# Kernel optimization log

Hardware: AMD Instinct MI355X
Metric: run time of the kernel (lower is better)

## Reference

```python
import jax, jax.numpy as jnp
import numpy as np

N_NODES = 100000


def _gcn_layer(x, src, dst, ew, norm_s, norm_d, W, b):
    # DGL GraphConv with edge weights, norm='both':
    # h_v = D_in(v)^-1/2 * sum_{(u,v) in E} w_uv * D_out(u)^-1/2 * x_u; then Linear.
    m = (x * norm_s[:, None])[src] * ew[:, None]        # [E, d] gather + weight
    agg = jax.ops.segment_sum(m, dst, num_segments=N_NODES)  # [N, d] scatter-add
    return (agg * norm_d[:, None]) @ W + b


def setup_inputs() -> dict:
    key = jax.random.key(0)
    ks = jax.random.split(key, 12)
    N, E, D, C = N_NODES, 1600000, 64, 32
    inp = {
        "x": jax.random.normal(ks[0], (N, D), jnp.float32),
        "src": jax.random.randint(ks[1], (E,), 0, N, jnp.int64),
        "dst": jax.random.randint(ks[2], (E,), 0, N, jnp.int64),
        "ew": jax.random.uniform(ks[3], (E,), jnp.float32),
    }
    s = 1.0 / np.sqrt(D)
    for i, k in zip(range(1, 5), ks[4:8]):
        inp[f"W{i}"] = jax.random.normal(k, (D, D), jnp.float32) * s
        inp[f"b{i}"] = jnp.zeros((D,), jnp.float32)
    inp["Wr"] = jax.random.normal(ks[8], (D, D), jnp.float32) * s
    inp["br"] = jnp.zeros((D,), jnp.float32)
    inp["Wo"] = jax.random.normal(ks[9], (D, C), jnp.float32) * s
    inp["bo"] = jnp.zeros((C,), jnp.float32)
    return inp


def reference(x, src, dst, ew, W1, b1, W2, b2, W3, b3, W4, b4, Wr, br, Wo, bo):
    ones = jnp.ones(src.shape, x.dtype)
    deg_out = jnp.clip(jax.ops.segment_sum(ones, src, num_segments=N_NODES), 1.0)
    deg_in = jnp.clip(jax.ops.segment_sum(ones, dst, num_segments=N_NODES), 1.0)
    norm_s = deg_out ** -0.5
    norm_d = deg_in ** -0.5

    res = x @ Wr + br
    h = jax.nn.relu(_gcn_layer(x, src, dst, ew, norm_s, norm_d, W1, b1))
    h = jax.nn.relu(_gcn_layer(h, src, dst, ew, norm_s, norm_d, W2, b2))
    h = jax.nn.relu(_gcn_layer(h, src, dst, ew, norm_s, norm_d, W3, b3))
    h = _gcn_layer(h, src, dst, ew, norm_s, norm_d, W4, b4)
    h = jax.nn.relu(h + res)
    return h @ Wo + bo
```

## Files before the change

### kernel.cpp

```cpp
#include <hip/hip_runtime.h>

#define NN 100000
#define D 64
#define G 4
#define RS 25000
#define NC 64
#define NB (G*NC)

typedef short bf16x8 __attribute__((ext_vector_type(8)));
typedef float f32x4 __attribute__((ext_vector_type(4)));

__device__ __forceinline__ float bf2f_lo(unsigned w) { return __uint_as_float(w << 16); }
__device__ __forceinline__ float bf2f_hi(unsigned w) { return __uint_as_float(w & 0xffff0000u); }
__device__ __forceinline__ unsigned short f2bf(float f) {
    unsigned u = __float_as_uint(f);
    return (unsigned short)((u + 0x7fffu + ((u >> 16) & 1u)) >> 16);
}
__device__ __forceinline__ unsigned pack2(float a, float b) {
    return (unsigned)f2bf(a) | ((unsigned)f2bf(b) << 16);
}

__global__ __launch_bounds__(1024) void k_hist(const int* __restrict__ src,
                                               const int* __restrict__ dst,
                                               unsigned* __restrict__ part, int E) {
    __shared__ unsigned h[RS];
    int b = blockIdx.x, t = threadIdx.x;
    int g = b >> 6, c = b & 63;
    int lo = g * RS;
    for (int i = t; i < RS; i += 1024) h[i] = 0;
    __syncthreads();
    int e0 = (int)((((long long)c * E / NC)) & ~3LL);
    int e1 = (c == NC - 1) ? E : (int)((((long long)(c + 1) * E / NC)) & ~3LL);
    int m = (e1 - e0) & ~4095;
    for (int e = e0 + t * 4; e < e0 + m; e += 4096) {
        int4 s4 = *(const int4*)(src + e);
        int4 d4 = *(const int4*)(dst + e);
        int v;
        v = s4.x - lo; if ((unsigned)v < RS) atomicAdd(&h[v], 1u);
        v = s4.y - lo; if ((unsigned)v < RS) atomicAdd(&h[v], 1u);
        v = s4.z - lo; if ((unsigned)v < RS) atomicAdd(&h[v], 1u);
        v = s4.w - lo; if ((unsigned)v < RS) atomicAdd(&h[v], 1u);
        v = d4.x - lo; if ((unsigned)v < RS) atomicAdd(&h[v], 0x10000u);
        v = d4.y - lo; if ((unsigned)v < RS) atomicAdd(&h[v], 0x10000u);
        v = d4.z - lo; if ((unsigned)v < RS) atomicAdd(&h[v], 0x10000u);
        v = d4.w - lo; if ((unsigned)v < RS) atomicAdd(&h[v], 0x10000u);
    }
    for (int e = e0 + m + t; e < e1; e += 1024) {
        int v = src[e] - lo; if ((unsigned)v < RS) atomicAdd(&h[v], 1u);
        v = dst[e] - lo;     if ((unsigned)v < RS) atomicAdd(&h[v], 0x10000u);
    }
    __syncthreads();
    unsigned* pb = part + (size_t)b * RS;
    for (int i = t; i < RS; i += 1024) pb[i] = h[i];
}

__global__ __launch_bounds__(1024) void k_scan1m(const unsigned* __restrict__ part,
                                                 float* __restrict__ ns, float* __restrict__ nd,
                                                 int* __restrict__ rowptr,
                                                 int* __restrict__ bsum, int n) {
    __shared__ int lds[1024];
    int t = threadIdx.x;
    int i = blockIdx.x * 1024 + t;
    int sv = 0, dv = 0;
    if (i < n) {
        int g = i / RS, off = i - g * RS;
        const unsigned* p = part + (size_t)(g * NC) * RS + off;
        #pragma unroll 8
        for (int c = 0; c < NC; ++c) {
            unsigned v = p[(size_t)c * RS];
            sv += (int)(v & 0xffffu);
            dv += (int)(v >> 16);
        }
        ns[i] = rsqrtf(fmaxf((float)sv, 1.0f));
        nd[i] = rsqrtf(fmaxf((float)dv, 1.0f));
    }
    lds[t] = dv;
    __syncthreads();
    for (int off = 1; off < 1024; off <<= 1) {
        int v = lds[t];
        int a = (t >= off) ? lds[t - off] : 0;
        __syncthreads();
        lds[t] = v + a;
        __syncthreads();
    }
    if (t == 1023) bsum[blockIdx.x] = lds[1023];
    if (i < n) rowptr[i] = lds[t] - dv;
}

__global__ void k_scan3c(int* __restrict__ rowptr, const int* __restrict__ bsum,
                         const unsigned* __restrict__ part, int* __restrict__ cur_part,
                         int n, int E, int nb) {
    __shared__ int sbs[128];
    int t = threadIdx.x;
    if (t < 128) sbs[t] = (t < nb) ? bsum[t] : 0;
    __syncthreads();
    for (int off = 1; off < 128; off <<= 1) {
        int v = 0, a = 0;
        if (t < 128) { v = sbs[t]; if (t >= off) a = sbs[t - off]; }
        __syncthreads();
        if (t < 128) sbs[t] = v + a;
        __syncthreads();
    }
    int i = blockIdx.x * blockDim.x + t;
    if (i == 0) rowptr[n] = E;
    if (i >= n) return;
    int blk = i >> 10;
    int base = (blk > 0) ? sbs[blk - 1] : 0;
    int r = rowptr[i] + base;
    rowptr[i] = r;
    int g = i / RS, off = i - g * RS;
    const unsigned* p = part + (size_t)(g * NC) * RS + off;
    int* cp = cur_part + (size_t)(g * NC) * RS + off;
    int run = r;
    #pragma unroll 8
    for (int c = 0; c < NC; ++c) {
        cp[(size_t)c * RS] = run;
        run += (int)(p[(size_t)c * RS] >> 16);
    }
}

__global__ __launch_bounds__(1024) void k_fillsort(const int* __restrict__ src,
                                                   const int* __restrict__ dst,
                                                   const float* __restrict__ ew,
                                                   const int* __restrict__ cur_part,
                                                   int2* __restrict__ cw, int E) {
    __shared__ int cur[RS];
    int b = blockIdx.x, t = threadIdx.x;
    int g = b >> 6, c = b & 63;
    int lo = g * RS;
    const int* cp = cur_part + (size_t)b * RS;
    for (int i = t; i < RS; i += 1024) cur[i] = cp[i];
    __syncthreads();
    int e0 = (int)((((long long)c * E / NC)) & ~3LL);
    int e1 = (c == NC - 1) ? E : (int)((((long long)(c + 1) * E / NC)) & ~3LL);
    int m = (e1 - e0) & ~4095;
    for (int e = e0 + t * 4; e < e0 + m; e += 4096) {
        int4 s4 = *(const int4*)(src + e);
        int4 d4 = *(const int4*)(dst + e);
        float4 w4 = *(const float4*)(ew + e);
        int d;
        d = d4.x - lo; if ((unsigned)d < RS) { int p = atomicAdd(&cur[d], 1); cw[p] = make_int2(s4.x, __float_as_int(w4.x)); }
        d = d4.y - lo; if ((unsigned)d < RS) { int p = atomicAdd(&cur[d], 1); cw[p] = make_int2(s4.y, __float_as_int(w4.y)); }
        d = d4.z - lo; if ((unsigned)d < RS) { int p = atomicAdd(&cur[d], 1); cw[p] = make_int2(s4.z, __float_as_int(w4.z)); }
        d = d4.w - lo; if ((unsigned)d < RS) { int p = atomicAdd(&cur[d], 1); cw[p] = make_int2(s4.w, __float_as_int(w4.w)); }
    }
    for (int e = e0 + m + t; e < e1; e += 1024) {
        int d = dst[e] - lo;
        if ((unsigned)d < RS) {
            int p = atomicAdd(&cur[d], 1);
            cw[p] = make_int2(src[e], __float_as_int(ew[e]));
        }
    }
}

__global__ void k_scale(const float* __restrict__ x, const float* __restrict__ ns,
                        unsigned short* __restrict__ xsb, int n16) {
    int i = blockIdx.x * blockDim.x + threadIdx.x;
    if (i < n16) {
        float s = ns[i >> 4];
        float4 v = ((const float4*)x)[i];
        ((uint2*)xsb)[i] = make_uint2(pack2(v.x * s, v.y * s), pack2(v.z * s, v.w * s));
    }
}

template<bool LAST>
__global__ void k_gather(const int* __restrict__ rowptr, const int2* __restrict__ cw,
                         const unsigned short* __restrict__ tmat,
                         const float* __restrict__ nd, const float* __restrict__ ns,
                         const float* __restrict__ bias,
                         const unsigned short* __restrict__ resb,
                         unsigned short* __restrict__ outb, int n, int E) {
    int node = blockIdx.x * (blockDim.x >> 5) + (threadIdx.x >> 5);
    int lane = threadIdx.x & 31;
    if (node >= n) return;
    int g = lane >> 3;
    int h = lane & 7;
    int beg = rowptr[node], end = rowptr[node + 1];
    float a0=0,a1=0,a2=0,a3=0,a4=0,a5=0,a6=0,a7=0;
    float c0=0,c1=0,c2=0,c3=0,c4=0,c5=0,c6=0,c7=0;
    for (int base = beg; base < end; base += 16) {
        int eA = base + g;
        int eB = eA + 4;
        int eC = eA + 8;
        int eD = eA + 12;
        int2 cvA = cw[min(eA, E - 1)];
        int2 cvB = cw[min(eB, E - 1)];
        int2 cvC = cw[min(eC, E - 1)];
        int2 cvD = cw[min(eD, E - 1)];
        float wA = (eA < end) ? __int_as_float(cvA.y) : 0.f;
        float wB = (eB < end) ? __int_as_float(cvB.y) : 0.f;
        float wC = (eC < end) ? __int_as_float(cvC.y) : 0.f;
        float wD = (eD < end) ? __int_as_float(cvD.y) : 0.f;
        uint4 rA = *((const uint4*)(tmat + (size_t)cvA.x * D) + h);
        uint4 rB = *((const uint4*)(tmat + (size_t)cvB.x * D) + h);
        uint4 rC = *((const uint4*)(tmat + (size_t)cvC.x * D) + h);
        uint4 rD = *((const uint4*)(tmat + (size_t)cvD.x * D) + h);
        a0 += wA * bf2f_lo(rA.x); a1 += wA * bf2f_hi(rA.x);
        a2 += wA * bf2f_lo(rA.y); a3 += wA * bf2f_hi(rA.y);
        a4 += wA * bf2f_lo(rA.z); a5 += wA * bf2f_hi(rA.z);
        a6 += wA * bf2f_lo(rA.w); a7 += wA * bf2f_hi(rA.w);
        c0 += wB * bf2f_lo(rB.x); c1 += wB * bf2f_hi(rB.x);
        c2 += wB * bf2f_lo(rB.y); c3 += wB * bf2f_hi(rB.y);
        c4 += wB * bf2f_lo(rB.z); c5 += wB * bf2f_hi(rB.z);
        c6 += wB * bf2f_lo(rB.w); c7 += wB * bf2f_hi(rB.w);
        a0 += wC * bf2f_lo(rC.x); a1 += wC * bf2f_hi(rC.x);
        a2 += wC * bf2f_lo(rC.y); a3 += wC * bf2f_hi(rC.y);
        a4 += wC * bf2f_lo(rC.z); a5 += wC * bf2f_hi(rC.z);
        a6 += wC * bf2f_lo(rC.w); a7 += wC * bf2f_hi(rC.w);
        c0 += wD * bf2f_lo(rD.x); c1 += wD * bf2f_hi(rD.x);
        c2 += wD * bf2f_lo(rD.y); c3 += wD * bf2f_hi(rD.y);
        c4 += wD * bf2f_lo(rD.z); c5 += wD * bf2f_hi(rD.z);
        c6 += wD * bf2f_lo(rD.w); c7 += wD * bf2f_hi(rD.w);
    }
    a0 += c0; a1 += c1; a2 += c2; a3 += c3;
    a4 += c4; a5 += c5; a6 += c6; a7 += c7;
    #pragma unroll
    for (int msk = 8; msk <= 16; msk <<= 1) {
        a0 += __shfl_xor(a0, msk); a1 += __shfl_xor(a1, msk);
        a2 += __shfl_xor(a2, msk); a3 += __shfl_xor(a3, msk);
        a4 += __shfl_xor(a4, msk); a5 += __shfl_xor(a5, msk);
        a6 += __shfl_xor(a6, msk); a7 += __shfl_xor(a7, msk);
    }
    float ndv = nd[node];
    float4 b0 = *(const float4*)(bias + 8 * h);
    float4 b1 = *(const float4*)(bias + 8 * h + 4);
    float v0 = ndv * a0 + b0.x, v1 = ndv * a1 + b0.y;
    float v2 = ndv * a2 + b0.z, v3 = ndv * a3 + b0.w;
    float v4 = ndv * a4 + b1.x, v5 = ndv * a5 + b1.y;
    float v6 = ndv * a6 + b1.z, v7 = ndv * a7 + b1.w;
    if (LAST) {
        uint4 r = *((const uint4*)(resb + (size_t)node * D) + h);
        v0 += bf2f_lo(r.x); v1 += bf2f_hi(r.x);
        v2 += bf2f_lo(r.y); v3 += bf2f_hi(r.y);
        v4 += bf2f_lo(r.z); v5 += bf2f_hi(r.z);
        v6 += bf2f_lo(r.w); v7 += bf2f_hi(r.w);
    }
    v0 = fmaxf(v0, 0.f); v1 = fmaxf(v1, 0.f); v2 = fmaxf(v2, 0.f); v3 = fmaxf(v3, 0.f);
    v4 = fmaxf(v4, 0.f); v5 = fmaxf(v5, 0.f); v6 = fmaxf(v6, 0.f); v7 = fmaxf(v7, 0.f);
    if (!LAST) {
        float s = ns[node];
        v0 *= s; v1 *= s; v2 *= s; v3 *= s; v4 *= s; v5 *= s; v6 *= s; v7 *= s;
    }
    if (g == 0) {
        uint4 o = make_uint4(pack2(v0, v1), pack2(v2, v3), pack2(v4, v5), pack2(v6, v7));
        *((uint4*)(outb + (size_t)node * D) + h) = o;
    }
}

template<int OUTD, bool BIAS, bool IN_BF16, bool OUT_BF16>
__global__ __launch_bounds__(256) void k_gemm(const void* __restrict__ in_,
                                              const float* __restrict__ W,
                                              const float* __restrict__ bias,
                                              void* __restrict__ out_, int n) {
    constexpr int NT = OUTD / 16;
    __shared__ unsigned short WT[OUTD][72];
    int t = threadIdx.x;
    for (int i = t; i < 64 * OUTD; i += 256) {
        int k = i / OUTD, nn = i % OUTD;
        WT[nn][k] = f2bf(W[i]);
    }
    __syncthreads();
    int w = t >> 6, lane = t & 63;
    int m = lane & 15, q = lane >> 4;
    int node0 = blockIdx.x * 64 + w * 16;
    int nodeA = min(node0 + m, n - 1);
    bf16x8 afr[2];
    if (IN_BF16) {
        const unsigned short* inb = (const unsigned short*)in_ + (size_t)nodeA * D;
        #pragma unroll
        for (int kc = 0; kc < 2; ++kc) {
            union { bf16x8 v; uint4 u; } tmp;
            tmp.u = *(const uint4*)(inb + kc * 32 + q * 8);
            afr[kc] = tmp.v;
        }
    } else {
        const float* inf = (const float*)in_ + (size_t)nodeA * D;
        #pragma unroll
        for (int kc = 0; kc < 2; ++kc) {
            float4 f0 = *(const float4*)(inf + kc * 32 + q * 8);
            float4 f1 = *(const float4*)(inf + kc * 32 + q * 8 + 4);
            union { bf16x8 v; unsigned short u[8]; } tmp;
            tmp.u[0] = f2bf(f0.x); tmp.u[1] = f2bf(f0.y);
            tmp.u[2] = f2bf(f0.z); tmp.u[3] = f2bf(f0.w);
            tmp.u[4] = f2bf(f1.x); tmp.u[5] = f2bf(f1.y);
            tmp.u[6] = f2bf(f1.z); tmp.u[7] = f2bf(f1.w);
            afr[kc] = tmp.v;
        }
    }
    #pragma unroll
    for (int nt = 0; nt < NT; ++nt) {
        f32x4 acc = {0.f, 0.f, 0.f, 0.f};
        #pragma unroll
        for (int kc = 0; kc < 2; ++kc) {
            union { bf16x8 v; uint4 u; } bfr;
            bfr.u = *(const uint4*)&WT[nt * 16 + m][kc * 32 + q * 8];
            acc = __builtin_amdgcn_mfma_f32_16x16x32_bf16(afr[kc], bfr.v, acc, 0, 0, 0);
        }
        int col = nt * 16 + m;
        float bb = BIAS ? bias[col] : 0.f;
        #pragma unroll
        for (int r = 0; r < 4; ++r) {
            int node = node0 + q * 4 + r;
            if (node < n) {
                float v = acc[r] + bb;
                if (OUT_BF16)
                    ((unsigned short*)out_)[(size_t)node * OUTD + col] = f2bf(v);
                else
                    ((float*)out_)[(size_t)node * OUTD + col] = v;
            }
        }
    }
}

static inline char* align_up(char* p, size_t a) {
    return (char*)(((uintptr_t)p + a - 1) & ~(uintptr_t)(a - 1));
}

extern "C" void kernel_launch(void* const* d_in, const int* in_sizes, int n_in,
                              void* d_out, int out_size, void* d_ws, size_t ws_size,
                              hipStream_t stream) {
    const float* x   = (const float*)d_in[0];
    const int*   src = (const int*)d_in[1];
    const int*   dst = (const int*)d_in[2];
    const float* ew  = (const float*)d_in[3];
    const float* Wl[4] = {(const float*)d_in[4], (const float*)d_in[6],
                          (const float*)d_in[8], (const float*)d_in[10]};
    const float* bl[4] = {(const float*)d_in[5], (const float*)d_in[7],
                          (const float*)d_in[9], (const float*)d_in[11]};
    const float* Wr = (const float*)d_in[12];
    const float* br = (const float*)d_in[13];
    const float* Wo = (const float*)d_in[14];
    const float* bo = (const float*)d_in[15];
    float* out = (float*)d_out;

    const int N = NN;
    const int E = in_sizes[1];

    char* p = (char*)d_ws;
    float* norm_s = (float*)p;            p = align_up(p + N * 4, 256);
    float* norm_d = (float*)p;            p = align_up(p + N * 4, 256);
    int*   rowptr = (int*)p;              p = align_up(p + (N + 1) * 4, 256);
    int*   bsum   = (int*)p;              p = align_up(p + 128 * 4, 256);
    int2*  cw     = (int2*)p;             p = align_up(p + (size_t)E * 8, 256);
    unsigned* part = (unsigned*)p;        p = align_up(p + (size_t)NB * RS * 4, 256);
    int* cur_part  = (int*)p;             p = align_up(p + (size_t)NB * RS * 4, 256);
    unsigned short* xs   = (unsigned short*)part;
    unsigned short* tmat = xs + (size_t)N * D;
    unsigned short* resb = (unsigned short*)cur_part;

    k_hist<<<NB, 1024, 0, stream>>>(src, dst, part, E);
    int nb = (N + 1023) / 1024;
    k_scan1m<<<nb, 1024, 0, stream>>>(part, norm_s, norm_d, rowptr, bsum, N);
    k_scan3c<<<(N + 255) / 256, 256, 0, stream>>>(rowptr, bsum, part, cur_part, N, E, nb);
    k_fillsort<<<NB, 1024, 0, stream>>>(src, dst, ew, cur_part, cw, E);

    k_scale<<<(N * 16 + 255) / 256, 256, 0, stream>>>(x, norm_s, xs, N * 16);
    k_gemm<64, true, false, true><<<(N + 63) / 64, 256, 0, stream>>>(x, Wr, br, resb, N);

    for (int l = 0; l < 4; ++l) {
        k_gemm<64, false, true, true><<<(N + 63) / 64, 256, 0, stream>>>(
            xs, Wl[l], nullptr, tmat, N);
        if (l < 3) {
            k_gather<false><<<(N + 7) / 8, 256, 0, stream>>>(
                rowptr, cw, tmat, norm_d, norm_s, bl[l], nullptr, xs, N, E);
        } else {
            k_gather<true><<<(N + 7) / 8, 256, 0, stream>>>(
                rowptr, cw, tmat, norm_d, nullptr, bl[l], resb, xs, N, E);
        }
    }
    k_gemm<32, true, true, false><<<(N + 63) / 64, 256, 0, stream>>>(xs, Wo, bo, out, N);
}
```

Measured before the change: 358.1 us.

## Pack per-chunk degree histograms into 8-bit counts and 16-bit relative cursors

```diff
diff --git a/kernel.cpp b/kernel.cpp
--- a/kernel.cpp
+++ b/kernel.cpp
@@ -2,9 +2,9 @@
 
 #define NN 100000
 #define D 64
-#define G 4
-#define RS 25000
-#define NC 64
+#define G 3
+#define RS 33334
+#define NC 85
 #define NB (G*NC)
 
 typedef short bf16x8 __attribute__((ext_vector_type(8)));
@@ -22,12 +22,12 @@
 
 __global__ __launch_bounds__(1024) void k_hist(const int* __restrict__ src,
                                                const int* __restrict__ dst,
-                                               unsigned* __restrict__ part, int E) {
-    __shared__ unsigned h[RS];
+                                               unsigned short* __restrict__ psd, int E) {
+    __shared__ unsigned h[RS / 2];
     int b = blockIdx.x, t = threadIdx.x;
-    int g = b >> 6, c = b & 63;
+    int g = b / NC, c = b - g * NC;
     int lo = g * RS;
-    for (int i = t; i < RS; i += 1024) h[i] = 0;
+    for (int i = t; i < RS / 2; i += 1024) h[i] = 0;
     __syncthreads();
     int e0 = (int)((((long long)c * E / NC)) & ~3LL);
     int e1 = (c == NC - 1) ? E : (int)((((long long)(c + 1) * E / NC)) & ~3LL);
@@ -36,25 +36,25 @@
         int4 s4 = *(const int4*)(src + e);
         int4 d4 = *(const int4*)(dst + e);
         int v;
-        v = s4.x - lo; if ((unsigned)v < RS) atomicAdd(&h[v], 1u);
-        v = s4.y - lo; if ((unsigned)v < RS) atomicAdd(&h[v], 1u);
-        v = s4.z - lo; if ((unsigned)v < RS) atomicAdd(&h[v], 1u);
-        v = s4.w - lo; if ((unsigned)v < RS) atomicAdd(&h[v], 1u);
-        v = d4.x - lo; if ((unsigned)v < RS) atomicAdd(&h[v], 0x10000u);
-        v = d4.y - lo; if ((unsigned)v < RS) atomicAdd(&h[v], 0x10000u);
-        v = d4.z - lo; if ((unsigned)v < RS) atomicAdd(&h[v], 0x10000u);
-        v = d4.w - lo; if ((unsigned)v < RS) atomicAdd(&h[v], 0x10000u);
+        v = s4.x - lo; if ((unsigned)v < RS) atomicAdd(&h[v >> 1], 1u << ((v & 1) * 16));
+        v = s4.y - lo; if ((unsigned)v < RS) atomicAdd(&h[v >> 1], 1u << ((v & 1) * 16));
+        v = s4.z - lo; if ((unsigned)v < RS) atomicAdd(&h[v >> 1], 1u << ((v & 1) * 16));
+        v = s4.w - lo; if ((unsigned)v < RS) atomicAdd(&h[v >> 1], 1u << ((v & 1) * 16));
+        v = d4.x - lo; if ((unsigned)v < RS) atomicAdd(&h[v >> 1], 1u << ((v & 1) * 16 + 8));
+        v = d4.y - lo; if ((unsigned)v < RS) atomicAdd(&h[v >> 1], 1u << ((v & 1) * 16 + 8));
+        v = d4.z - lo; if ((unsigned)v < RS) atomicAdd(&h[v >> 1], 1u << ((v & 1) * 16 + 8));
+        v = d4.w - lo; if ((unsigned)v < RS) atomicAdd(&h[v >> 1], 1u << ((v & 1) * 16 + 8));
     }
     for (int e = e0 + m + t; e < e1; e += 1024) {
-        int v = src[e] - lo; if ((unsigned)v < RS) atomicAdd(&h[v], 1u);
-        v = dst[e] - lo;     if ((unsigned)v < RS) atomicAdd(&h[v], 0x10000u);
-    }
-    __syncthreads();
-    unsigned* pb = part + (size_t)b * RS;
-    for (int i = t; i < RS; i += 1024) pb[i] = h[i];
-}
-
-__global__ __launch_bounds__(1024) void k_scan1m(const unsigned* __restrict__ part,
+        int v = src[e] - lo; if ((unsigned)v < RS) atomicAdd(&h[v >> 1], 1u << ((v & 1) * 16));
+        v = dst[e] - lo;     if ((unsigned)v < RS) atomicAdd(&h[v >> 1], 1u << ((v & 1) * 16 + 8));
+    }
+    __syncthreads();
+    unsigned* pb = (unsigned*)(psd + (size_t)b * RS);
+    for (int i = t; i < RS / 2; i += 1024) pb[i] = h[i];
+}
+
+__global__ __launch_bounds__(1024) void k_scan1m(const unsigned short* __restrict__ psd,
                                                  float* __restrict__ ns, float* __restrict__ nd,
                                                  int* __restrict__ rowptr,
                                                  int* __restrict__ bsum, int n) {
@@ -64,12 +64,12 @@
     int sv = 0, dv = 0;
     if (i < n) {
         int g = i / RS, off = i - g * RS;
-        const unsigned* p = part + (size_t)(g * NC) * RS + off;
-        #pragma unroll 8
+        const unsigned short* p = psd + (size_t)(g * NC) * RS + off;
+        #pragma unroll 5
         for (int c = 0; c < NC; ++c) {
             unsigned v = p[(size_t)c * RS];
-            sv += (int)(v & 0xffffu);
-            dv += (int)(v >> 16);
+            sv += (int)(v & 0xffu);
+            dv += (int)(v >> 8);
         }
         ns[i] = rsqrtf(fmaxf((float)sv, 1.0f));
         nd[i] = rsqrtf(fmaxf((float)dv, 1.0f));
@@ -88,7 +88,8 @@
 }
 
 __global__ void k_scan3c(int* __restrict__ rowptr, const int* __restrict__ bsum,
-                         const unsigned* __restrict__ part, int* __restrict__ cur_part,
+                         const unsigned short* __restrict__ psd,
+                         unsigned short* __restrict__ cur16,
                          int n, int E, int nb) {
     __shared__ int sbs[128];
     int t = threadIdx.x;
@@ -109,27 +110,28 @@
     int r = rowptr[i] + base;
     rowptr[i] = r;
     int g = i / RS, off = i - g * RS;
-    const unsigned* p = part + (size_t)(g * NC) * RS + off;
-    int* cp = cur_part + (size_t)(g * NC) * RS + off;
-    int run = r;
-    #pragma unroll 8
+    const unsigned short* p = psd + (size_t)(g * NC) * RS + off;
+    unsigned short* cp = cur16 + (size_t)(g * NC) * RS + off;
+    int run = 0;
+    #pragma unroll 5
     for (int c = 0; c < NC; ++c) {
-        cp[(size_t)c * RS] = run;
-        run += (int)(p[(size_t)c * RS] >> 16);
+        cp[(size_t)c * RS] = (unsigned short)run;
+        run += (int)(p[(size_t)c * RS] >> 8);
     }
 }
 
 __global__ __launch_bounds__(1024) void k_fillsort(const int* __restrict__ src,
                                                    const int* __restrict__ dst,
                                                    const float* __restrict__ ew,
-                                                   const int* __restrict__ cur_part,
+                                                   const int* __restrict__ rowptr,
+                                                   const unsigned short* __restrict__ cur16,
                                                    int2* __restrict__ cw, int E) {
     __shared__ int cur[RS];
     int b = blockIdx.x, t = threadIdx.x;
-    int g = b >> 6, c = b & 63;
+    int g = b / NC, c = b - g * NC;
     int lo = g * RS;
-    const int* cp = cur_part + (size_t)b * RS;
-    for (int i = t; i < RS; i += 1024) cur[i] = cp[i];
+    const unsigned short* c16 = cur16 + (size_t)b * RS;
+    for (int i = t; i < RS; i += 1024) cur[i] = rowptr[lo + i] + (int)c16[i];
     __syncthreads();
     int e0 = (int)((((long long)c * E / NC)) & ~3LL);
     int e1 = (c == NC - 1) ? E : (int)((((long long)(c + 1) * E / NC)) & ~3LL);
@@ -339,20 +341,20 @@
     char* p = (char*)d_ws;
     float* norm_s = (float*)p;            p = align_up(p + N * 4, 256);
     float* norm_d = (float*)p;            p = align_up(p + N * 4, 256);
-    int*   rowptr = (int*)p;              p = align_up(p + (N + 1) * 4, 256);
+    int*   rowptr = (int*)p;              p = align_up(p + (size_t)(G * RS + 80) * 4, 256);
     int*   bsum   = (int*)p;              p = align_up(p + 128 * 4, 256);
     int2*  cw     = (int2*)p;             p = align_up(p + (size_t)E * 8, 256);
-    unsigned* part = (unsigned*)p;        p = align_up(p + (size_t)NB * RS * 4, 256);
-    int* cur_part  = (int*)p;             p = align_up(p + (size_t)NB * RS * 4, 256);
-    unsigned short* xs   = (unsigned short*)part;
+    unsigned short* psd   = (unsigned short*)p; p = align_up(p + (size_t)NB * RS * 2, 256);
+    unsigned short* cur16 = (unsigned short*)p; p = align_up(p + (size_t)NB * RS * 2, 256);
+    unsigned short* resb  = (unsigned short*)p; p = align_up(p + (size_t)N * D * 2, 256);
+    unsigned short* xs   = psd;
     unsigned short* tmat = xs + (size_t)N * D;
-    unsigned short* resb = (unsigned short*)cur_part;
-
-    k_hist<<<NB, 1024, 0, stream>>>(src, dst, part, E);
+
+    k_hist<<<NB, 1024, 0, stream>>>(src, dst, psd, E);
     int nb = (N + 1023) / 1024;
-    k_scan1m<<<nb, 1024, 0, stream>>>(part, norm_s, norm_d, rowptr, bsum, N);
-    k_scan3c<<<(N + 255) / 256, 256, 0, stream>>>(rowptr, bsum, part, cur_part, N, E, nb);
-    k_fillsort<<<NB, 1024, 0, stream>>>(src, dst, ew, cur_part, cw, E);
+    k_scan1m<<<nb, 1024, 0, stream>>>(psd, norm_s, norm_d, rowptr, bsum, N);
+    k_scan3c<<<(N + 255) / 256, 256, 0, stream>>>(rowptr, bsum, psd, cur16, N, E, nb);
+    k_fillsort<<<NB, 1024, 0, stream>>>(src, dst, ew, rowptr, cur16, cw, E);
 
     k_scale<<<(N * 16 + 255) / 256, 256, 0, stream>>>(x, norm_s, xs, N * 16);
     k_gemm<64, true, false, true><<<(N + 63) / 64, 256, 0, stream>>>(x, Wr, br, resb, N);
```

New measurement: 357.9 us. No clear change (-0.1%).
